# Kernel optimization log

Measured on AMD Instinct MI355X. Metric: run time of the kernel, lower is better.

The kernel has to match this reference:

```python
import jax, jax.numpy as jnp
import numpy as np

C = 32          # in_channels = out_channels = groups
K = 3           # kernel_size
STRIDE = 2
PAD = 1
DIL = 1
EPS = 1e-20


def _depthwise_convT(x, w):
    """Equivalent of torch.F.conv_transpose2d(x, w, groups=C, stride=STRIDE,
    padding=PAD, dilation=DIL) with w of shape (C, 1, K, K).
    Implemented as an lhs-dilated conv with a spatially flipped kernel."""
    w_f = w[:, :, ::-1, ::-1]
    pad = DIL * (K - 1) - PAD  # = 1 for K=3, PAD=1, DIL=1
    return jax.lax.conv_general_dilated(
        x, w_f,
        window_strides=(1, 1),
        padding=[(pad, pad), (pad, pad)],
        lhs_dilation=(STRIDE, STRIDE),
        rhs_dilation=(DIL, DIL),
        dimension_numbers=('NCHW', 'OIHW', 'NCHW'),
        feature_group_count=C)


def setup_inputs() -> dict:
    key = jax.random.key(0)
    k = jax.random.split(key, 7)
    B, H, W = 2, 176, 608
    # depths/confidences are positive (rand); gy is signed (randn)
    d = jax.random.uniform(k[0], (B, C, H, W), dtype=jnp.float32) + 0.5
    cd = jax.random.uniform(k[1], (B, C, H, W), dtype=jnp.float32)
    gy = jax.random.normal(k[2], (B, C, H, W), dtype=jnp.float32)
    cgy = jax.random.uniform(k[3], (B, C, H, W), dtype=jnp.float32)
    w_prop_raw = jax.random.normal(k[4], (1, C, 1, 1), dtype=jnp.float32)
    spatial_weight_raw = jax.random.normal(k[5], (C, 1, K, K), dtype=jnp.float32)
    bias = 0.01 * jax.random.normal(k[6], (1, C, 1, 1), dtype=jnp.float32)
    return {"d": d, "cd": cd, "gy": gy, "cgy": cgy,
            "w_prop_raw": w_prop_raw,
            "spatial_weight_raw": spatial_weight_raw,
            "bias": bias}


def reference(d, cd, gy, cgy, w_prop_raw, spatial_weight_raw, bias):
    # EnforcePos('softplus') on both learned weights
    w_prop = jax.nn.softplus(w_prop_raw)          # (1, C, 1, 1)
    sw = jax.nn.softplus(spatial_weight_raw)      # (C, 1, K, K)

    # roll-based vertical neighbor gather with edge confidence zeroing
    d_up = jnp.roll(d, 1, axis=2)
    cd_up = jnp.roll(cd, 1, axis=2).at[:, :, 0, :].set(0.0)
    d_down = jnp.roll(d, -1, axis=2)
    cd_down = jnp.roll(cd, -1, axis=2).at[:, :, -1, :].set(0.0)

    cgy_from_ds = cd_up * cd_up
    height = (cd_up * d_up + cd_down * d_down) / (cd_up + cd_down)
    gy_from_ds = (d_down - d_up) / 2.0 / height

    gy_f = (w_prop * cgy * gy + cgy_from_ds * gy_from_ds) / (w_prop * cgy + cgy_from_ds)
    cgy_f = (w_prop * cgy + cgy_from_ds) / (w_prop + 1.0)

    nom = _depthwise_convT(cgy_f * gy_f, sw)
    denom = _depthwise_convT(cgy_f, sw)
    cdenom = _depthwise_convT(jnp.ones_like(cgy_f), sw)

    # original adds bias twice: once unconditionally, once under use_bias
    gy_out = nom / (denom + EPS) + bias + bias
    cgy_out = denom / (cdenom + EPS)
    return gy_out / STRIDE, cgy_out
```

## Files before the change

### kernel.cpp

```cpp
#include <hip/hip_runtime.h>
#include <math.h>

#define B_   2
#define C_   32
#define H_   176
#define W_   608
#define HO_  351
#define WO_  1215
#define PLANE_O (HO_ * WO_)
#define OUT1_O  (B_ * C_ * PLANE_O)
#define EPS_ 1e-20f
#define NTH  512
#define CSTRIDE 16
#define W4   (W_ / 4)

typedef float f4_t __attribute__((ext_vector_type(4)));

__device__ __forceinline__ float softplus_f(float x) {
    return fmaxf(x, 0.0f) + log1pf(expf(-fabsf(x)));
}

extern "C" __global__ void precompute_consts(const float* __restrict__ wpr,
                                             const float* __restrict__ swr,
                                             const float* __restrict__ bias,
                                             float* __restrict__ cc)
{
    const int c = threadIdx.x;
    if (c >= C_) return;
    float sw[9];
#pragma unroll
    for (int k = 0; k < 9; ++k) sw[k] = softplus_f(swr[c * 9 + k]);
    const float wp = softplus_f(wpr[c]);
    float* o = cc + c * CSTRIDE;
#pragma unroll
    for (int k = 0; k < 9; ++k) o[k] = sw[k];
    o[9]  = wp;
    o[10] = 1.0f / (wp + 1.0f);
    o[11] = bias[c];
    o[12] = 1.0f / (sw[4] + EPS_);
    o[13] = 1.0f / (sw[3] + sw[5] + EPS_);
    o[14] = 1.0f / (sw[1] + sw[7] + EPS_);
    o[15] = 1.0f / (sw[0] + sw[2] + sw[6] + sw[8] + EPS_);
}

extern "C" __global__ __launch_bounds__(NTH)
void structn_rows(const float* __restrict__ d,
                  const float* __restrict__ cd,
                  const float* __restrict__ gy,
                  const float* __restrict__ cgy,
                  const float* __restrict__ cc,
                  float* __restrict__ out)
{
    __shared__ float s_n[5 * W_];
    __shared__ float s_c[5 * W_];

    const int g     = blockIdx.x;
    const int plane = blockIdx.y;
    const int c     = plane & (C_ - 1);

    const float* __restrict__ ch = cc + c * CSTRIDE;
    const float sw0 = ch[0], sw1 = ch[1], sw2 = ch[2];
    const float sw3 = ch[3], sw4 = ch[4], sw5 = ch[5];
    const float sw6 = ch[6], sw7 = ch[7], sw8 = ch[8];
    const float wp      = ch[9];
    const float inv_wp1 = ch[10];
    const float bv      = ch[11];
    const float icd_ee  = ch[12];
    const float icd_eo  = ch[13];
    const float icd_oe  = ch[14];
    const float icd_oo  = ch[15];

    const int r0  = g * 4;
    const int nrf = (r0 + 4 <= H_ - 1) ? 5 : (H_ - r0);

    const int pbase = plane * (H_ * W_);
    const float* __restrict__ dP  = d   + pbase;
    const float* __restrict__ cdP = cd  + pbase;
    const float* __restrict__ gyP = gy  + pbase;
    const float* __restrict__ cgP = cgy + pbase;

    const int ntask = nrf * W4;
    for (int idx = threadIdx.x; idx < ntask; idx += NTH) {
        const int rf = idx / W4;
        const int iw = (idx - rf * W4) << 2;
        const int iy = r0 + rf;
        const int up = (iy == 0)      ? (H_ - 1) : iy - 1;
        const int dn = (iy == H_ - 1) ? 0        : iy + 1;
        const float mu = (iy > 0)      ? 1.0f : 0.0f;
        const float md = (iy < H_ - 1) ? 1.0f : 0.0f;

        const f4_t du = *(const f4_t*)(dP  + up * W_ + iw);
        const f4_t dd = *(const f4_t*)(dP  + dn * W_ + iw);
        const f4_t cu = *(const f4_t*)(cdP + up * W_ + iw);
        const f4_t cn = *(const f4_t*)(cdP + dn * W_ + iw);
        const f4_t gg = *(const f4_t*)(gyP + iy * W_ + iw);
        const f4_t cg = *(const f4_t*)(cgP + iy * W_ + iw);

        f4_t sn4, sc4;
#pragma unroll
        for (int e = 0; e < 4; ++e) {
            const float cuv = cu[e] * mu;
            const float cnv = cn[e] * md;
            const float cfd = cuv * cuv;
            const float rs  = __builtin_amdgcn_rcpf(fmaf(cuv, du[e], cnv * dd[e]));
            const float gfd = 0.5f * (dd[e] - du[e]) * (cuv + cnv) * rs;
            const float num = fmaf(wp * cg[e], gg[e], cfd * gfd);
            const float den = fmaf(wp, cg[e], cfd);
            sn4[e] = num * inv_wp1;
            sc4[e] = den * inv_wp1;
        }
        *(f4_t*)(s_n + rf * W_ + iw) = sn4;
        *(f4_t*)(s_c + rf * W_ + iw) = sc4;
    }
    __syncthreads();

    const int w    = threadIdx.x >> 6;
    const int lane = threadIdx.x & 63;
    const int oy   = g * 8 + w;
    if (oy >= HO_) return;

    const int p = w & 1;
    const int lrA = p ? ((w - 1) >> 1) : (w >> 1);
    const float* __restrict__ snA = s_n + lrA * W_;
    const float* __restrict__ scA = s_c + lrA * W_;
    const float* __restrict__ snB = p ? (snA + W_) : snA;
    const float* __restrict__ scB = p ? (scA + W_) : scA;

    const int ro0 = plane * PLANE_O + oy * WO_;
    float* __restrict__ o0 = out + ro0;
    float* __restrict__ o1 = out + OUT1_O + ro0;

    const int h  = (4 - (ro0 & 3)) & 3;
    const int n4 = (WO_ - h) >> 2;
    if (lane < 3) {
        const int ox = (lane < h) ? lane : (h + (n4 << 2) + lane - h);
        const int q  = ox & 1;
        float den, nom, icd;
        if (p == 0) {
            if (q == 0) {
                const int j = ox >> 1;
                den = scA[j] * sw4;  nom = snA[j] * sw4;  icd = icd_ee;
            } else {
                const int j = (ox - 1) >> 1;
                den = scA[j] * sw5 + scA[j + 1] * sw3;
                nom = snA[j] * sw5 + snA[j + 1] * sw3;  icd = icd_eo;
            }
        } else {
            if (q == 0) {
                const int j = ox >> 1;
                den = scA[j] * sw7 + scB[j] * sw1;
                nom = snA[j] * sw7 + snB[j] * sw1;  icd = icd_oe;
            } else {
                const int j = (ox - 1) >> 1;
                den = scA[j] * sw8 + scA[j + 1] * sw6 + scB[j] * sw2 + scB[j + 1] * sw0;
                nom = snA[j] * sw8 + snA[j + 1] * sw6 + snB[j] * sw2 + snB[j + 1] * sw0;
                icd = icd_oo;
            }
        }
        o0[ox] = fmaf(0.5f * nom, __builtin_amdgcn_rcpf(den + EPS_), bv);
        o1[ox] = den * icd;
    }

    const int patB = h & 1;
    if (p == 0) {
        if (!patB) {
            for (int k = lane; k < n4; k += 64) {
                const int c0 = h + (k << 2), j0 = c0 >> 1;
                const float a0 = snA[j0], a1 = snA[j0 + 1], a2 = snA[j0 + 2];
                const float x0 = scA[j0], x1 = scA[j0 + 1], x2 = scA[j0 + 2];
                const float d0 = x0 * sw4,            n0 = a0 * sw4;
                const float d1 = x0 * sw5 + x1 * sw3, n1 = a0 * sw5 + a1 * sw3;
                const float d2 = x1 * sw4,            n2 = a1 * sw4;
                const float d3 = x1 * sw5 + x2 * sw3, n3 = a1 * sw5 + a2 * sw3;
                f4_t gv, qv;
                gv.x = fmaf(0.5f * n0, __builtin_amdgcn_rcpf(d0 + EPS_), bv);
                gv.y = fmaf(0.5f * n1, __builtin_amdgcn_rcpf(d1 + EPS_), bv);
                gv.z = fmaf(0.5f * n2, __builtin_amdgcn_rcpf(d2 + EPS_), bv);
                gv.w = fmaf(0.5f * n3, __builtin_amdgcn_rcpf(d3 + EPS_), bv);
                qv.x = d0 * icd_ee; qv.y = d1 * icd_eo;
                qv.z = d2 * icd_ee; qv.w = d3 * icd_eo;
                *(f4_t*)(o0 + c0) = gv;
                *(f4_t*)(o1 + c0) = qv;
            }
        } else {
            for (int k = lane; k < n4; k += 64) {
                const int c0 = h + (k << 2), j0 = c0 >> 1;
                const float a0 = snA[j0], a1 = snA[j0 + 1], a2 = snA[j0 + 2];
                const float x0 = scA[j0], x1 = scA[j0 + 1], x2 = scA[j0 + 2];
                const float d0 = x0 * sw5 + x1 * sw3, n0 = a0 * sw5 + a1 * sw3;
                const float d1 = x1 * sw4,            n1 = a1 * sw4;
                const float d2 = x1 * sw5 + x2 * sw3, n2 = a1 * sw5 + a2 * sw3;
                const float d3 = x2 * sw4,            n3 = a2 * sw4;
                f4_t gv, qv;
                gv.x = fmaf(0.5f * n0, __builtin_amdgcn_rcpf(d0 + EPS_), bv);
                gv.y = fmaf(0.5f * n1, __builtin_amdgcn_rcpf(d1 + EPS_), bv);
                gv.z = fmaf(0.5f * n2, __builtin_amdgcn_rcpf(d2 + EPS_), bv);
                gv.w = fmaf(0.5f * n3, __builtin_amdgcn_rcpf(d3 + EPS_), bv);
                qv.x = d0 * icd_eo; qv.y = d1 * icd_ee;
                qv.z = d2 * icd_eo; qv.w = d3 * icd_ee;
                *(f4_t*)(o0 + c0) = gv;
                *(f4_t*)(o1 + c0) = qv;
            }
        }
    } else {
        if (!patB) {
            for (int k = lane; k < n4; k += 64) {
                const int c0 = h + (k << 2), j0 = c0 >> 1;
                const float a0 = snA[j0], a1 = snA[j0 + 1], a2 = snA[j0 + 2];
                const float x0 = scA[j0], x1 = scA[j0 + 1], x2 = scA[j0 + 2];
                const float b0 = snB[j0], b1 = snB[j0 + 1], b2 = snB[j0 + 2];
                const float y0 = scB[j0], y1 = scB[j0 + 1], y2 = scB[j0 + 2];
                const float d0 = x0 * sw7 + y0 * sw1;
                const float n0 = a0 * sw7 + b0 * sw1;
                const float d1 = x0 * sw8 + x1 * sw6 + y0 * sw2 + y1 * sw0;
                const float n1 = a0 * sw8 + a1 * sw6 + b0 * sw2 + b1 * sw0;
                const float d2 = x1 * sw7 + y1 * sw1;
                const float n2 = a1 * sw7 + b1 * sw1;
                const float d3 = x1 * sw8 + x2 * sw6 + y1 * sw2 + y2 * sw0;
                const float n3 = a1 * sw8 + a2 * sw6 + b1 * sw2 + b2 * sw0;
                f4_t gv, qv;
                gv.x = fmaf(0.5f * n0, __builtin_amdgcn_rcpf(d0 + EPS_), bv);
                gv.y = fmaf(0.5f * n1, __builtin_amdgcn_rcpf(d1 + EPS_), bv);
                gv.z = fmaf(0.5f * n2, __builtin_amdgcn_rcpf(d2 + EPS_), bv);
                gv.w = fmaf(0.5f * n3, __builtin_amdgcn_rcpf(d3 + EPS_), bv);
                qv.x = d0 * icd_oe; qv.y = d1 * icd_oo;
                qv.z = d2 * icd_oe; qv.w = d3 * icd_oo;
                *(f4_t*)(o0 + c0) = gv;
                *(f4_t*)(o1 + c0) = qv;
            }
        } else {
            for (int k = lane; k < n4; k += 64) {
                const int c0 = h + (k << 2), j0 = c0 >> 1;
                const float a0 = snA[j0], a1 = snA[j0 + 1], a2 = snA[j0 + 2];
                const float x0 = scA[j0], x1 = scA[j0 + 1], x2 = scA[j0 + 2];
                const float b0 = snB[j0], b1 = snB[j0 + 1], b2 = snB[j0 + 2];
                const float y0 = scB[j0], y1 = scB[j0 + 1], y2 = scB[j0 + 2];
                const float d0 = x0 * sw8 + x1 * sw6 + y0 * sw2 + y1 * sw0;
                const float n0 = a0 * sw8 + a1 * sw6 + b0 * sw2 + b1 * sw0;
                const float d1 = x1 * sw7 + y1 * sw1;
                const float n1 = a1 * sw7 + b1 * sw1;
                const float d2 = x1 * sw8 + x2 * sw6 + y1 * sw2 + y2 * sw0;
                const float n2 = a1 * sw8 + a2 * sw6 + b1 * sw2 + b2 * sw0;
                const float d3 = x2 * sw7 + y2 * sw1;
                const float n3 = a2 * sw7 + b2 * sw1;
                f4_t gv, qv;
                gv.x = fmaf(0.5f * n0, __builtin_amdgcn_rcpf(d0 + EPS_), bv);
                gv.y = fmaf(0.5f * n1, __builtin_amdgcn_rcpf(d1 + EPS_), bv);
                gv.z = fmaf(0.5f * n2, __builtin_amdgcn_rcpf(d2 + EPS_), bv);
                gv.w = fmaf(0.5f * n3, __builtin_amdgcn_rcpf(d3 + EPS_), bv);
                qv.x = d0 * icd_oo; qv.y = d1 * icd_oe;
                qv.z = d2 * icd_oo; qv.w = d3 * icd_oe;
                *(f4_t*)(o0 + c0) = gv;
                *(f4_t*)(o1 + c0) = qv;
            }
        }
    }
}

extern "C" void kernel_launch(void* const* d_in, const int* in_sizes, int n_in,
                              void* d_out, int out_size, void* d_ws, size_t ws_size,
                              hipStream_t stream) {
    const float* d    = (const float*)d_in[0];
    const float* cd   = (const float*)d_in[1];
    const float* gy   = (const float*)d_in[2];
    const float* cgy  = (const float*)d_in[3];
    const float* wpr  = (const float*)d_in[4];
    const float* swr  = (const float*)d_in[5];
    const float* bias = (const float*)d_in[6];
    float* out = (float*)d_out;
    float* cc  = (float*)d_ws;

    precompute_consts<<<1, 64, 0, stream>>>(wpr, swr, bias, cc);

    dim3 grid(44, B_ * C_);
    structn_rows<<<grid, NTH, 0, stream>>>(d, cd, gy, cgy, cc, out);
}
```

Baseline: 85.77 us.

## Split LDS rows into even/odd planes, fuse constant precompute, use nontemporal stores

Removes the separate precompute_consts launch and has every block compute the softplus constants inline. The intermediate rows in shared memory are stored as even/odd deinterleaved arrays, so the output loop reads with unit stride per lane, and the parity-specialized loops collapse into one loop per row parity using selects. Output stores become nontemporal, and launch_bounds gains a min-blocks hint. This trades a small amount of redundant transcendental work per block for one fewer kernel launch and fewer LDS bank conflicts.

Result: faster. 73.81 us (-13.9%).

```diff
diff --git a/kernel.cpp b/kernel.cpp
--- a/kernel.cpp
+++ b/kernel.cpp
@@ -11,64 +11,45 @@
 #define OUT1_O  (B_ * C_ * PLANE_O)
 #define EPS_ 1e-20f
 #define NTH  512
-#define CSTRIDE 16
 #define W4   (W_ / 4)
+#define HW_  304
 
 typedef float f4_t __attribute__((ext_vector_type(4)));
+typedef float f2_t __attribute__((ext_vector_type(2)));
 
 __device__ __forceinline__ float softplus_f(float x) {
     return fmaxf(x, 0.0f) + log1pf(expf(-fabsf(x)));
 }
 
-extern "C" __global__ void precompute_consts(const float* __restrict__ wpr,
-                                             const float* __restrict__ swr,
-                                             const float* __restrict__ bias,
-                                             float* __restrict__ cc)
-{
-    const int c = threadIdx.x;
-    if (c >= C_) return;
-    float sw[9];
-#pragma unroll
-    for (int k = 0; k < 9; ++k) sw[k] = softplus_f(swr[c * 9 + k]);
-    const float wp = softplus_f(wpr[c]);
-    float* o = cc + c * CSTRIDE;
-#pragma unroll
-    for (int k = 0; k < 9; ++k) o[k] = sw[k];
-    o[9]  = wp;
-    o[10] = 1.0f / (wp + 1.0f);
-    o[11] = bias[c];
-    o[12] = 1.0f / (sw[4] + EPS_);
-    o[13] = 1.0f / (sw[3] + sw[5] + EPS_);
-    o[14] = 1.0f / (sw[1] + sw[7] + EPS_);
-    o[15] = 1.0f / (sw[0] + sw[2] + sw[6] + sw[8] + EPS_);
-}
-
-extern "C" __global__ __launch_bounds__(NTH)
+extern "C" __global__ __launch_bounds__(NTH, 8)
 void structn_rows(const float* __restrict__ d,
                   const float* __restrict__ cd,
                   const float* __restrict__ gy,
                   const float* __restrict__ cgy,
-                  const float* __restrict__ cc,
+                  const float* __restrict__ wpr,
+                  const float* __restrict__ swr,
+                  const float* __restrict__ bias,
                   float* __restrict__ out)
 {
-    __shared__ float s_n[5 * W_];
-    __shared__ float s_c[5 * W_];
+    __shared__ float s_nE[5 * HW_];
+    __shared__ float s_nO[5 * HW_];
+    __shared__ float s_cE[5 * HW_];
+    __shared__ float s_cO[5 * HW_];
 
     const int g     = blockIdx.x;
     const int plane = blockIdx.y;
     const int c     = plane & (C_ - 1);
 
-    const float* __restrict__ ch = cc + c * CSTRIDE;
-    const float sw0 = ch[0], sw1 = ch[1], sw2 = ch[2];
-    const float sw3 = ch[3], sw4 = ch[4], sw5 = ch[5];
-    const float sw6 = ch[6], sw7 = ch[7], sw8 = ch[8];
-    const float wp      = ch[9];
-    const float inv_wp1 = ch[10];
-    const float bv      = ch[11];
-    const float icd_ee  = ch[12];
-    const float icd_eo  = ch[13];
-    const float icd_oe  = ch[14];
-    const float icd_oo  = ch[15];
+    float sw[9];
+#pragma unroll
+    for (int k = 0; k < 9; ++k) sw[k] = softplus_f(swr[c * 9 + k]);
+    const float wp      = softplus_f(wpr[c]);
+    const float inv_wp1 = 1.0f / (wp + 1.0f);
+    const float bv      = bias[c];
+    const float icd_ee  = 1.0f / (sw[4] + EPS_);
+    const float icd_eo  = 1.0f / (sw[3] + sw[5] + EPS_);
+    const float icd_oe  = 1.0f / (sw[1] + sw[7] + EPS_);
+    const float icd_oo  = 1.0f / (sw[0] + sw[2] + sw[6] + sw[8] + EPS_);
 
     const int r0  = g * 4;
     const int nrf = (r0 + 4 <= H_ - 1) ? 5 : (H_ - r0);
@@ -109,8 +90,12 @@
             sn4[e] = num * inv_wp1;
             sc4[e] = den * inv_wp1;
         }
-        *(f4_t*)(s_n + rf * W_ + iw) = sn4;
-        *(f4_t*)(s_c + rf * W_ + iw) = sc4;
+        const int eo = rf * HW_ + (iw >> 1);
+        f2_t v;
+        v[0] = sn4[0]; v[1] = sn4[2];  *(f2_t*)(s_nE + eo) = v;
+        v[0] = sn4[1]; v[1] = sn4[3];  *(f2_t*)(s_nO + eo) = v;
+        v[0] = sc4[0]; v[1] = sc4[2];  *(f2_t*)(s_cE + eo) = v;
+        v[0] = sc4[1]; v[1] = sc4[3];  *(f2_t*)(s_cO + eo) = v;
     }
     __syncthreads();
 
@@ -119,12 +104,8 @@
     const int oy   = g * 8 + w;
     if (oy >= HO_) return;
 
-    const int p = w & 1;
-    const int lrA = p ? ((w - 1) >> 1) : (w >> 1);
-    const float* __restrict__ snA = s_n + lrA * W_;
-    const float* __restrict__ scA = s_c + lrA * W_;
-    const float* __restrict__ snB = p ? (snA + W_) : snA;
-    const float* __restrict__ scB = p ? (scA + W_) : scA;
+    const int p   = w & 1;
+    const int lrA = w >> 1;
 
     const int ro0 = plane * PLANE_O + oy * WO_;
     float* __restrict__ o0 = out + ro0;
@@ -132,129 +113,146 @@
 
     const int h  = (4 - (ro0 & 3)) & 3;
     const int n4 = (WO_ - h) >> 2;
-    if (lane < 3) {
-        const int ox = (lane < h) ? lane : (h + (n4 << 2) + lane - h);
-        const int q  = ox & 1;
-        float den, nom, icd;
-        if (p == 0) {
-            if (q == 0) {
+    const int q  = h & 1;
+    const int r  = (h >> 1) & 1;
+
+    const float icdC = p ? icd_oe : icd_ee;
+    const float icdO = p ? icd_oo : icd_eo;
+    const float i0 = q ? icdO : icdC;
+    const float i1 = q ? icdC : icdO;
+
+    const float* __restrict__ nAE = s_nE + lrA * HW_;
+    const float* __restrict__ nAO = s_nO + lrA * HW_;
+    const float* __restrict__ cAE = s_cE + lrA * HW_;
+    const float* __restrict__ cAO = s_cO + lrA * HW_;
+
+#define VAL(E, O, j) (((j) & 1) ? (O)[((j) - 1) >> 1] : (E)[(j) >> 1])
+
+    if (p == 0) {
+        if (lane < 3) {
+            const int ox = (lane < h) ? lane : (h + (n4 << 2) + lane - h);
+            float den, nom, icd;
+            if ((ox & 1) == 0) {
                 const int j = ox >> 1;
-                den = scA[j] * sw4;  nom = snA[j] * sw4;  icd = icd_ee;
+                den = VAL(cAE, cAO, j) * sw[4];
+                nom = VAL(nAE, nAO, j) * sw[4];
+                icd = icd_ee;
             } else {
                 const int j = (ox - 1) >> 1;
-                den = scA[j] * sw5 + scA[j + 1] * sw3;
-                nom = snA[j] * sw5 + snA[j + 1] * sw3;  icd = icd_eo;
+                den = VAL(cAE, cAO, j) * sw[5] + VAL(cAE, cAO, j + 1) * sw[3];
+                nom = VAL(nAE, nAO, j) * sw[5] + VAL(nAE, nAO, j + 1) * sw[3];
+                icd = icd_eo;
             }
-        } else {
-            if (q == 0) {
+            o0[ox] = fmaf(0.5f * nom, __builtin_amdgcn_rcpf(den + EPS_), bv);
+            o1[ox] = den * icd;
+        }
+        const float* pa0 = r ? nAO : nAE;
+        const float* pa1 = r ? nAE + 1 : nAO;
+        const float* pa2 = r ? nAO + 1 : nAE + 1;
+        const float* px0 = r ? cAO : cAE;
+        const float* px1 = r ? cAE + 1 : cAO;
+        const float* px2 = r ? cAO + 1 : cAE + 1;
+
+        for (int k = lane; k < n4; k += 64) {
+            const float a0 = pa0[k], a1 = pa1[k], a2 = pa2[k];
+            const float x0 = px0[k], x1 = px1[k], x2 = px2[k];
+            const float dC0 = x0 * sw[4], dC1 = x1 * sw[4], dC2 = x2 * sw[4];
+            const float nC0 = a0 * sw[4], nC1 = a1 * sw[4], nC2 = a2 * sw[4];
+            const float dF0 = x0 * sw[5] + x1 * sw[3];
+            const float dF1 = x1 * sw[5] + x2 * sw[3];
+            const float nF0 = a0 * sw[5] + a1 * sw[3];
+            const float nF1 = a1 * sw[5] + a2 * sw[3];
+
+            const float d0 = q ? dF0 : dC0, n0 = q ? nF0 : nC0;
+            const float d1 = q ? dC1 : dF0, n1 = q ? nC1 : nF0;
+            const float d2 = q ? dF1 : dC1, n2 = q ? nF1 : nC1;
+            const float d3 = q ? dC2 : dF1, n3 = q ? nC2 : nF1;
+
+            f4_t gv, qv;
+            gv[0] = fmaf(0.5f * n0, __builtin_amdgcn_rcpf(d0 + EPS_), bv);
+            gv[1] = fmaf(0.5f * n1, __builtin_amdgcn_rcpf(d1 + EPS_), bv);
+            gv[2] = fmaf(0.5f * n2, __builtin_amdgcn_rcpf(d2 + EPS_), bv);
+            gv[3] = fmaf(0.5f * n3, __builtin_amdgcn_rcpf(d3 + EPS_), bv);
+            qv[0] = d0 * i0; qv[1] = d1 * i1; qv[2] = d2 * i0; qv[3] = d3 * i1;
+
+            const int c0 = h + (k << 2);
+            __builtin_nontemporal_store(gv, (f4_t*)(o0 + c0));
+            __builtin_nontemporal_store(qv, (f4_t*)(o1 + c0));
+        }
+    } else {
+        const float* __restrict__ nBE = nAE + HW_;
+        const float* __restrict__ nBO = nAO + HW_;
+        const float* __restrict__ cBE = cAE + HW_;
+        const float* __restrict__ cBO = cAO + HW_;
+
+        if (lane < 3) {
+            const int ox = (lane < h) ? lane : (h + (n4 << 2) + lane - h);
+            float den, nom, icd;
+            if ((ox & 1) == 0) {
                 const int j = ox >> 1;
-                den = scA[j] * sw7 + scB[j] * sw1;
-                nom = snA[j] * sw7 + snB[j] * sw1;  icd = icd_oe;
+                den = VAL(cAE, cAO, j) * sw[7] + VAL(cBE, cBO, j) * sw[1];
+                nom = VAL(nAE, nAO, j) * sw[7] + VAL(nBE, nBO, j) * sw[1];
+                icd = icd_oe;
             } else {
                 const int j = (ox - 1) >> 1;
-                den = scA[j] * sw8 + scA[j + 1] * sw6 + scB[j] * sw2 + scB[j + 1] * sw0;
-                nom = snA[j] * sw8 + snA[j + 1] * sw6 + snB[j] * sw2 + snB[j + 1] * sw0;
+                den = VAL(cAE, cAO, j) * sw[8] + VAL(cAE, cAO, j + 1) * sw[6]
+                    + VAL(cBE, cBO, j) * sw[2] + VAL(cBE, cBO, j + 1) * sw[0];
+                nom = VAL(nAE, nAO, j) * sw[8] + VAL(nAE, nAO, j + 1) * sw[6]
+                    + VAL(nBE, nBO, j) * sw[2] + VAL(nBE, nBO, j + 1) * sw[0];
                 icd = icd_oo;
             }
-        }
-        o0[ox] = fmaf(0.5f * nom, __builtin_amdgcn_rcpf(den + EPS_), bv);
-        o1[ox] = den * icd;
+            o0[ox] = fmaf(0.5f * nom, __builtin_amdgcn_rcpf(den + EPS_), bv);
+            o1[ox] = den * icd;
+        }
+
+        const float* pa0 = r ? nAO : nAE;
+        const float* pa1 = r ? nAE + 1 : nAO;
+        const float* pa2 = r ? nAO + 1 : nAE + 1;
+        const float* px0 = r ? cAO : cAE;
+        const float* px1 = r ? cAE + 1 : cAO;
+        const float* px2 = r ? cAO + 1 : cAE + 1;
+        const float* pb0 = r ? nBO : nBE;
+        const float* pb1 = r ? nBE + 1 : nBO;
+        const float* pb2 = r ? nBO + 1 : nBE + 1;
+        const float* py0 = r ? cBO : cBE;
+        const float* py1 = r ? cBE + 1 : cBO;
+        const float* py2 = r ? cBO + 1 : cBE + 1;
+
+        for (int k = lane; k < n4; k += 64) {
+            const float a0 = pa0[k], a1 = pa1[k], a2 = pa2[k];
+            const float x0 = px0[k], x1 = px1[k], x2 = px2[k];
+            const float b0 = pb0[k], b1 = pb1[k], b2 = pb2[k];
+            const float y0 = py0[k], y1 = py1[k], y2 = py2[k];
+
+            const float dC0 = x0 * sw[7] + y0 * sw[1];
+            const float dC1 = x1 * sw[7] + y1 * sw[1];
+            const float dC2 = x2 * sw[7] + y2 * sw[1];
+            const float nC0 = a0 * sw[7] + b0 * sw[1];
+            const float nC1 = a1 * sw[7] + b1 * sw[1];
+            const float nC2 = a2 * sw[7] + b2 * sw[1];
+            const float dF0 = x0 * sw[8] + x1 * sw[6] + y0 * sw[2] + y1 * sw[0];
+            const float dF1 = x1 * sw[8] + x2 * sw[6] + y1 * sw[2] + y2 * sw[0];
+            const float nF0 = a0 * sw[8] + a1 * sw[6] + b0 * sw[2] + b1 * sw[0];
+            const float nF1 = a1 * sw[8] + a2 * sw[6] + b1 * sw[2] + b2 * sw[0];
+
+            const float d0 = q ? dF0 : dC0, n0 = q ? nF0 : nC0;
+            const float d1 = q ? dC1 : dF0, n1 = q ? nC1 : nF0;
+            const float d2 = q ? dF1 : dC1, n2 = q ? nF1 : nC1;
+            const float d3 = q ? dC2 : dF1, n3 = q ? nC2 : nF1;
+
+            f4_t gv, qv;
+            gv[0] = fmaf(0.5f * n0, __builtin_amdgcn_rcpf(d0 + EPS_), bv);
+            gv[1] = fmaf(0.5f * n1, __builtin_amdgcn_rcpf(d1 + EPS_), bv);
+            gv[2] = fmaf(0.5f * n2, __builtin_amdgcn_rcpf(d2 + EPS_), bv);
+            gv[3] = fmaf(0.5f * n3, __builtin_amdgcn_rcpf(d3 + EPS_), bv);
+            qv[0] = d0 * i0; qv[1] = d1 * i1; qv[2] = d2 * i0; qv[3] = d3 * i1;
+
+            const int c0 = h + (k << 2);
+            __builtin_nontemporal_store(gv, (f4_t*)(o0 + c0));
+            __builtin_nontemporal_store(qv, (f4_t*)(o1 + c0));
+        }
     }
-
-    const int patB = h & 1;
-    if (p == 0) {
-        if (!patB) {
-            for (int k = lane; k < n4; k += 64) {
-                const int c0 = h + (k << 2), j0 = c0 >> 1;
-                const float a0 = snA[j0], a1 = snA[j0 + 1], a2 = snA[j0 + 2];
-                const float x0 = scA[j0], x1 = scA[j0 + 1], x2 = scA[j0 + 2];
-                const float d0 = x0 * sw4,            n0 = a0 * sw4;
-                const float d1 = x0 * sw5 + x1 * sw3, n1 = a0 * sw5 + a1 * sw3;
-                const float d2 = x1 * sw4,            n2 = a1 * sw4;
-                const float d3 = x1 * sw5 + x2 * sw3, n3 = a1 * sw5 + a2 * sw3;
-                f4_t gv, qv;
-                gv.x = fmaf(0.5f * n0, __builtin_amdgcn_rcpf(d0 + EPS_), bv);
-                gv.y = fmaf(0.5f * n1, __builtin_amdgcn_rcpf(d1 + EPS_), bv);
-                gv.z = fmaf(0.5f * n2, __builtin_amdgcn_rcpf(d2 + EPS_), bv);
-                gv.w = fmaf(0.5f * n3, __builtin_amdgcn_rcpf(d3 + EPS_), bv);
-                qv.x = d0 * icd_ee; qv.y = d1 * icd_eo;
-                qv.z = d2 * icd_ee; qv.w = d3 * icd_eo;
-                *(f4_t*)(o0 + c0) = gv;
-                *(f4_t*)(o1 + c0) = qv;
-            }
-        } else {
-            for (int k = lane; k < n4; k += 64) {
-                const int c0 = h + (k << 2), j0 = c0 >> 1;
-                const float a0 = snA[j0], a1 = snA[j0 + 1], a2 = snA[j0 + 2];
-                const float x0 = scA[j0], x1 = scA[j0 + 1], x2 = scA[j0 + 2];
-                const float d0 = x0 * sw5 + x1 * sw3, n0 = a0 * sw5 + a1 * sw3;
-                const float d1 = x1 * sw4,            n1 = a1 * sw4;
-                const float d2 = x1 * sw5 + x2 * sw3, n2 = a1 * sw5 + a2 * sw3;
-                const float d3 = x2 * sw4,            n3 = a2 * sw4;
-                f4_t gv, qv;
-                gv.x = fmaf(0.5f * n0, __builtin_amdgcn_rcpf(d0 + EPS_), bv);
-                gv.y = fmaf(0.5f * n1, __builtin_amdgcn_rcpf(d1 + EPS_), bv);
-                gv.z = fmaf(0.5f * n2, __builtin_amdgcn_rcpf(d2 + EPS_), bv);
-                gv.w = fmaf(0.5f * n3, __builtin_amdgcn_rcpf(d3 + EPS_), bv);
-                qv.x = d0 * icd_eo; qv.y = d1 * icd_ee;
-                qv.z = d2 * icd_eo; qv.w = d3 * icd_ee;
-                *(f4_t*)(o0 + c0) = gv;
-                *(f4_t*)(o1 + c0) = qv;
-            }
-        }
-    } else {
-        if (!patB) {
-            for (int k = lane; k < n4; k += 64) {
-                const int c0 = h + (k << 2), j0 = c0 >> 1;
-                const float a0 = snA[j0], a1 = snA[j0 + 1], a2 = snA[j0 + 2];
-                const float x0 = scA[j0], x1 = scA[j0 + 1], x2 = scA[j0 + 2];
-                const float b0 = snB[j0], b1 = snB[j0 + 1], b2 = snB[j0 + 2];
-                const float y0 = scB[j0], y1 = scB[j0 + 1], y2 = scB[j0 + 2];
-                const float d0 = x0 * sw7 + y0 * sw1;
-                const float n0 = a0 * sw7 + b0 * sw1;
-                const float d1 = x0 * sw8 + x1 * sw6 + y0 * sw2 + y1 * sw0;
-                const float n1 = a0 * sw8 + a1 * sw6 + b0 * sw2 + b1 * sw0;
-                const float d2 = x1 * sw7 + y1 * sw1;
-                const float n2 = a1 * sw7 + b1 * sw1;
-                const float d3 = x1 * sw8 + x2 * sw6 + y1 * sw2 + y2 * sw0;
-                const float n3 = a1 * sw8 + a2 * sw6 + b1 * sw2 + b2 * sw0;
-                f4_t gv, qv;
-                gv.x = fmaf(0.5f * n0, __builtin_amdgcn_rcpf(d0 + EPS_), bv);
-                gv.y = fmaf(0.5f * n1, __builtin_amdgcn_rcpf(d1 + EPS_), bv);
-                gv.z = fmaf(0.5f * n2, __builtin_amdgcn_rcpf(d2 + EPS_), bv);
-                gv.w = fmaf(0.5f * n3, __builtin_amdgcn_rcpf(d3 + EPS_), bv);
-                qv.x = d0 * icd_oe; qv.y = d1 * icd_oo;
-                qv.z = d2 * icd_oe; qv.w = d3 * icd_oo;
-                *(f4_t*)(o0 + c0) = gv;
-                *(f4_t*)(o1 + c0) = qv;
-            }
-        } else {
-            for (int k = lane; k < n4; k += 64) {
-                const int c0 = h + (k << 2), j0 = c0 >> 1;
-                const float a0 = snA[j0], a1 = snA[j0 + 1], a2 = snA[j0 + 2];
-                const float x0 = scA[j0], x1 = scA[j0 + 1], x2 = scA[j0 + 2];
-                const float b0 = snB[j0], b1 = snB[j0 + 1], b2 = snB[j0 + 2];
-                const float y0 = scB[j0], y1 = scB[j0 + 1], y2 = scB[j0 + 2];
-                const float d0 = x0 * sw8 + x1 * sw6 + y0 * sw2 + y1 * sw0;
-                const float n0 = a0 * sw8 + a1 * sw6 + b0 * sw2 + b1 * sw0;
-                const float d1 = x1 * sw7 + y1 * sw1;
-                const float n1 = a1 * sw7 + b1 * sw1;
-                const float d2 = x1 * sw8 + x2 * sw6 + y1 * sw2 + y2 * sw0;
-                const float n2 = a1 * sw8 + a2 * sw6 + b1 * sw2 + b2 * sw0;
-                const float d3 = x2 * sw7 + y2 * sw1;
-                const float n3 = a2 * sw7 + b2 * sw1;
-                f4_t gv, qv;
-                gv.x = fmaf(0.5f * n0, __builtin_amdgcn_rcpf(d0 + EPS_), bv);
-                gv.y = fmaf(0.5f * n1, __builtin_amdgcn_rcpf(d1 + EPS_), bv);
-                gv.z = fmaf(0.5f * n2, __builtin_amdgcn_rcpf(d2 + EPS_), bv);
-                gv.w = fmaf(0.5f * n3, __builtin_amdgcn_rcpf(d3 + EPS_), bv);
-                qv.x = d0 * icd_oo; qv.y = d1 * icd_oe;
-                qv.z = d2 * icd_oo; qv.w = d3 * icd_oe;
-                *(f4_t*)(o0 + c0) = gv;
-                *(f4_t*)(o1 + c0) = qv;
-            }
-        }
-    }
+#undef VAL
 }
 
 extern "C" void kernel_launch(void* const* d_in, const int* in_sizes, int n_in,
@@ -268,10 +266,7 @@
     const float* swr  = (const float*)d_in[5];
     const float* bias = (const float*)d_in[6];
     float* out = (float*)d_out;
-    float* cc  = (float*)d_ws;
-
-    precompute_consts<<<1, 64, 0, stream>>>(wpr, swr, bias, cc);
 
     dim3 grid(44, B_ * C_);
-    structn_rows<<<grid, NTH, 0, stream>>>(d, cd, gy, cgy, cc, out);
+    structn_rows<<<grid, NTH, 0, stream>>>(d, cd, gy, cgy, wpr, swr, bias, out);
 }
```
